# Kernel tuning notes

Hardware: AMD Instinct MI355X
Metric: run time of the kernel (lower is better)

The kernel has to match this reference:

```python
import jax, jax.numpy as jnp
import numpy as np

NEG_SLOPE = 0.2

def gat_layer(x, W, al, ar, src, dst, n_dst):
    # x: [Ns, Fin]; W: [Fin, H*D]; al/ar: [H, D]; src/dst: [E]
    H, D = al.shape
    h = (x @ W).reshape(-1, H, D)          # [Ns, H, D]
    h_dst = h[:n_dst]                       # dst nodes are prefix of src nodes (DGL block)
    el = (h * al).sum(-1)                   # [Ns, H]
    er = (h_dst * ar).sum(-1)               # [Nd, H]
    e = jax.nn.leaky_relu(el[src] + er[dst], NEG_SLOPE)  # [E, H]
    m = jax.ops.segment_max(e, dst, num_segments=n_dst)  # stable edge-softmax
    a = jnp.exp(e - m[dst])
    s = jax.ops.segment_sum(a, dst, num_segments=n_dst)
    alpha = a / s[dst]                      # [E, H]
    msg = h[src] * alpha[:, :, None]        # [E, H, D]
    out = jax.ops.segment_sum(msg, dst, num_segments=n_dst)  # [Nd, H, D]
    return out.reshape(n_dst, H * D)


def setup_inputs() -> dict:
    key = jax.random.key(0)
    ks = jax.random.split(key, 16)
    N0, N1, N2, N3 = 200000, 100000, 50000, 25000
    E0, E1, E2 = 1000000, 500000, 250000
    Fin, Dh, H, C = 256, 64, 3, 40
    inp = {}
    inp['x'] = jax.random.normal(ks[0], (N0, Fin), jnp.float32)
    inp['src0'] = jax.random.randint(ks[1], (E0,), 0, N0, jnp.int32)
    inp['dst0'] = jnp.sort(jax.random.randint(ks[2], (E0,), 0, N1, jnp.int32))
    inp['src1'] = jax.random.randint(ks[3], (E1,), 0, N1, jnp.int32)
    inp['dst1'] = jnp.sort(jax.random.randint(ks[4], (E1,), 0, N2, jnp.int32))
    inp['src2'] = jax.random.randint(ks[5], (E2,), 0, N2, jnp.int32)
    inp['dst2'] = jnp.sort(jax.random.randint(ks[6], (E2,), 0, N3, jnp.int32))
    sc = lambda f: np.float32(1.0 / np.sqrt(f))
    inp['W0'] = jax.random.normal(ks[7], (Fin, H * Dh), jnp.float32) * sc(Fin)
    inp['al0'] = jax.random.normal(ks[8], (H, Dh), jnp.float32) * sc(Dh)
    inp['ar0'] = jax.random.normal(ks[9], (H, Dh), jnp.float32) * sc(Dh)
    inp['W1'] = jax.random.normal(ks[10], (H * Dh, H * Dh), jnp.float32) * sc(H * Dh)
    inp['al1'] = jax.random.normal(ks[11], (H, Dh), jnp.float32) * sc(Dh)
    inp['ar1'] = jax.random.normal(ks[12], (H, Dh), jnp.float32) * sc(Dh)
    inp['W2'] = jax.random.normal(ks[13], (H * Dh, C), jnp.float32) * sc(H * Dh)
    inp['al2'] = jax.random.normal(ks[14], (1, C), jnp.float32) * sc(C)
    inp['ar2'] = jax.random.normal(ks[15], (1, C), jnp.float32) * sc(C)
    return inp


def reference(x, src0, dst0, src1, dst1, src2, dst2,
              W0, al0, ar0, W1, al1, ar1, W2, al2, ar2):
    N1, N2, N3 = 100000, 50000, 25000
    h = gat_layer(x, W0, al0, ar0, src0, dst0, N1)
    h = jax.nn.relu(h)  # dropout is identity in eval/deterministic mode
    h = gat_layer(h, W1, al1, ar1, src1, dst1, N2)
    h = jax.nn.relu(h)
    out = gat_layer(h, W2, al2, ar2, src2, dst2, N3)  # [N3, n_classes]
    return out
```

## Files before the change

kernel.cpp:

```cpp
#include <hip/hip_runtime.h>
#include <math.h>

#define DEV_INLINE __device__ __forceinline__

typedef __attribute__((ext_vector_type(8))) short short8v;
typedef __attribute__((ext_vector_type(4))) float float4v;

DEV_INLINE unsigned short f2bf_rtn(float f) {
  unsigned u = __float_as_uint(f);
  u += 0x7FFFu + ((u >> 16) & 1u);
  return (unsigned short)(u >> 16);
}
DEV_INLINE float bf2f(unsigned short s) { return __uint_as_float(((unsigned)s) << 16); }

DEV_INLINE int soff(int row, int oct) { return row * 32 + ((oct ^ (row & 3)) << 3); }

__global__ void conv_w_all(const float* __restrict__ W0, const float* __restrict__ W1,
                           const float* __restrict__ W2, short* __restrict__ w0h,
                           short* __restrict__ w0l, short* __restrict__ w1h,
                           short* __restrict__ w1l, short* __restrict__ w2h,
                           short* __restrict__ w2l) {
  const int S0 = 256 * 192, S1 = 192 * 192, S2 = 192 * 40;
  int idx = blockIdx.x * 256 + threadIdx.x;
  const float* W; short *Wh, *Wl; int K;
  if (idx < S0) { W = W0; Wh = w0h; Wl = w0l; K = 256; }
  else if (idx < S0 + S1) { idx -= S0; W = W1; Wh = w1h; Wl = w1l; K = 192; }
  else if (idx < S0 + S1 + S2) { idx -= S0 + S1; W = W2; Wh = w2h; Wl = w2l; K = 192; }
  else return;
  int n = idx / K, k = idx - n * K;
  int N = (W == W0 || W == W1) ? 192 : 40;
  float w = W[(size_t)k * N + n];
  unsigned short h = f2bf_rtn(w);
  Wh[idx] = (short)h;
  Wl[idx] = (short)f2bf_rtn(w - bf2f(h));
}

__global__ void csr_all(const int* __restrict__ d0, const int* __restrict__ d1,
                        const int* __restrict__ d2, int* __restrict__ o0,
                        int* __restrict__ o1, int* __restrict__ o2,
                        int E0, int E1, int E2, int n1, int n2, int n3) {
  int i = blockIdx.x * 256 + threadIdx.x;
  const int* dst; int* off; int E, nd;
  if (i < E0) { dst = d0; off = o0; E = E0; nd = n1; }
  else if (i < E0 + E1) { i -= E0; dst = d1; off = o1; E = E1; nd = n2; }
  else if (i < E0 + E1 + E2) { i -= E0 + E1; dst = d2; off = o2; E = E2; nd = n3; }
  else return;
  int d = dst[i];
  int p = (i == 0) ? -1 : dst[i - 1];
  for (int q = p + 1; q <= d; ++q) off[q] = i;
  if (i == E - 1)
    for (int q = d + 1; q <= nd; ++q) off[q] = E;
}

template <int NT, int H>
__global__ __launch_bounds__(256) void gemm_fused(
    const float* __restrict__ A, const short* __restrict__ Bth,
    const short* __restrict__ Btl, const float* __restrict__ al,
    const float* __restrict__ ar, float* __restrict__ C,
    float* __restrict__ el, float* __restrict__ er,
    int M, int N, int K, int n_dst) {
  constexpr int BN = NT * 16;
  constexpr int BREP = (BN + 63) / 64;
  constexpr int TPH = NT / H;
  __shared__ short As_h[128 * 32], As_l[128 * 32];
  __shared__ short Bs_h[BN * 32], Bs_l[BN * 32];
  const int tid = threadIdx.x;
  const int w = tid >> 6, lane = tid & 63;
  const int quad = lane >> 4, l16 = lane & 15;
  const int m0 = blockIdx.x * 128;

  float4v acc[2][NT];
#pragma unroll
  for (int mt = 0; mt < 2; ++mt)
#pragma unroll
    for (int nt = 0; nt < NT; ++nt)
#pragma unroll
      for (int r = 0; r < 4; ++r) acc[mt][nt][r] = 0.f;

  const int sr = tid >> 2;
  const int oct = tid & 3;

  for (int k0 = 0; k0 < K; k0 += 32) {
    float4 a0[2], a1[2];
#pragma unroll
    for (int p = 0; p < 2; ++p) {
      int gr = m0 + sr + p * 64;
      if (gr < M) {
        const float* ap = A + (size_t)gr * K + k0 + oct * 8;
        a0[p] = *(const float4*)ap;
        a1[p] = *(const float4*)(ap + 4);
      } else {
        a0[p] = make_float4(0.f, 0.f, 0.f, 0.f);
        a1[p] = a0[p];
      }
    }
    short8v bh[BREP], bl[BREP];
#pragma unroll
    for (int q = 0; q < BREP; ++q) {
      int n = sr + q * 64;
      if (n < BN) {
        if (n < N) {
          bh[q] = *(const short8v*)(Bth + (size_t)n * K + k0 + oct * 8);
          bl[q] = *(const short8v*)(Btl + (size_t)n * K + k0 + oct * 8);
        } else {
#pragma unroll
          for (int j = 0; j < 8; ++j) { bh[q][j] = 0; bl[q][j] = 0; }
        }
      }
    }
    __syncthreads();
#pragma unroll
    for (int p = 0; p < 2; ++p) {
      int r = sr + p * 64;
      float vs[8] = {a0[p].x, a0[p].y, a0[p].z, a0[p].w,
                     a1[p].x, a1[p].y, a1[p].z, a1[p].w};
      short8v hv, lv;
#pragma unroll
      for (int j = 0; j < 8; ++j) {
        unsigned short h = f2bf_rtn(vs[j]);
        hv[j] = (short)h;
        lv[j] = (short)f2bf_rtn(vs[j] - bf2f(h));
      }
      *(short8v*)(As_h + soff(r, oct)) = hv;
      *(short8v*)(As_l + soff(r, oct)) = lv;
    }
#pragma unroll
    for (int q = 0; q < BREP; ++q) {
      int n = sr + q * 64;
      if (n < BN) {
        *(short8v*)(Bs_h + soff(n, oct)) = bh[q];
        *(short8v*)(Bs_l + soff(n, oct)) = bl[q];
      }
    }
    __syncthreads();
    short8v afh[2], afl[2];
#pragma unroll
    for (int mt = 0; mt < 2; ++mt) {
      int row = w * 32 + mt * 16 + l16;
      afh[mt] = *(const short8v*)(As_h + soff(row, quad));
      afl[mt] = *(const short8v*)(As_l + soff(row, quad));
    }
#pragma unroll
    for (int nt = 0; nt < NT; ++nt) {
      int col = nt * 16 + l16;
      short8v bfh = *(const short8v*)(Bs_h + soff(col, quad));
      short8v bfl = *(const short8v*)(Bs_l + soff(col, quad));
#pragma unroll
      for (int mt = 0; mt < 2; ++mt) {
        acc[mt][nt] = __builtin_amdgcn_mfma_f32_16x16x32_bf16(afh[mt], bfh, acc[mt][nt], 0, 0, 0);
        acc[mt][nt] = __builtin_amdgcn_mfma_f32_16x16x32_bf16(afh[mt], bfl, acc[mt][nt], 0, 0, 0);
        acc[mt][nt] = __builtin_amdgcn_mfma_f32_16x16x32_bf16(afl[mt], bfh, acc[mt][nt], 0, 0, 0);
      }
    }
  }

  float av[NT], rv[NT];
#pragma unroll
  for (int nt = 0; nt < NT; ++nt) {
    int col = nt * 16 + l16;
    av[nt] = (col < N) ? al[col] : 0.f;
    rv[nt] = (col < N) ? ar[col] : 0.f;
  }
#pragma unroll
  for (int mt = 0; mt < 2; ++mt)
#pragma unroll
    for (int r = 0; r < 4; ++r) {
      int gm = m0 + w * 32 + mt * 16 + quad * 4 + r;
      if (gm >= M) continue;
      float pl[H], pr[H];
#pragma unroll
      for (int h = 0; h < H; ++h) { pl[h] = 0.f; pr[h] = 0.f; }
#pragma unroll
      for (int nt = 0; nt < NT; ++nt) {
        int h = nt / TPH;
        pl[h] = fmaf(acc[mt][nt][r], av[nt], pl[h]);
        pr[h] = fmaf(acc[mt][nt][r], rv[nt], pr[h]);
      }
#pragma unroll
      for (int h = 0; h < H; ++h) {
#pragma unroll
        for (int o = 8; o >= 1; o >>= 1) {
          pl[h] += __shfl_xor(pl[h], o, 16);
          pr[h] += __shfl_xor(pr[h], o, 16);
        }
      }
      if (l16 == 0) {
#pragma unroll
        for (int h = 0; h < H; ++h) {
          el[gm * H + h] = pl[h];
          if (gm < n_dst) er[gm * H + h] = pr[h];
        }
      }
#pragma unroll
      for (int nt = 0; nt < NT; ++nt) {
        int col = nt * 16 + l16;
        if (col < N) C[(size_t)gm * N + col] = acc[mt][nt][r];
      }
    }
}

template <int H, int D, bool RELU>
__global__ __launch_bounds__(256) void agg2_kernel(
    const float* __restrict__ hsrc, const float* __restrict__ el,
    const float* __restrict__ er, const int* __restrict__ src,
    const int* __restrict__ off, float* __restrict__ out, int n_dst) {
  constexpr int F = H * D;
  constexpr int NP = (F + 63) / 64;
  __shared__ float wbuf[16][16][H];
  __shared__ int sbuf[16][16];
  const int g = threadIdx.x >> 4, l = threadIdx.x & 15;
  const int d = blockIdx.x * 16 + g;
  if (d >= n_dst) return;
  const int lo = off[d], hi = off[d + 1];

  if (hi <= lo) {
#pragma unroll
    for (int p = 0; p < NP; ++p) {
      int c4 = (p * 16 + l) * 4;
      if (c4 < F) *(float4*)(out + (size_t)d * F + c4) = make_float4(0.f, 0.f, 0.f, 0.f);
    }
    return;
  }

  float erv[H], s_part[H];
#pragma unroll
  for (int h = 0; h < H; ++h) {
    erv[h] = er[d * H + h];
    s_part[h] = 0.f;
  }
  float4 acc[NP];
#pragma unroll
  for (int p = 0; p < NP; ++p) acc[p] = make_float4(0.f, 0.f, 0.f, 0.f);

  for (int base = lo; base < hi; base += 16) {
    const int i = base + l;
    const bool valid = i < hi;
    const int sid = valid ? src[i] : 0;
#pragma unroll
    for (int h = 0; h < H; ++h) {
      float e = 0.f;
      if (valid) {
        e = el[sid * H + h] + erv[h];
        e = e > 0.f ? e : 0.2f * e;
        e = __expf(e);
      }
      s_part[h] += e;
      wbuf[g][l][h] = e;
    }
    sbuf[g][l] = sid;

    const int cnt = min(16, hi - base);
    int sj = sbuf[g][0];
    float4 hv[NP], hn[NP];
#pragma unroll
    for (int p = 0; p < NP; ++p) {
      int c4 = (p * 16 + l) * 4;
      hv[p] = (c4 < F) ? *(const float4*)(hsrc + (size_t)sj * F + c4)
                       : make_float4(0.f, 0.f, 0.f, 0.f);
    }
    for (int ei = 0; ei < cnt; ++ei) {
      if (ei + 1 < cnt) {
        int sj2 = sbuf[g][ei + 1];
#pragma unroll
        for (int p = 0; p < NP; ++p) {
          int c4 = (p * 16 + l) * 4;
          hn[p] = (c4 < F) ? *(const float4*)(hsrc + (size_t)sj2 * F + c4)
                           : make_float4(0.f, 0.f, 0.f, 0.f);
        }
      }
#pragma unroll
      for (int p = 0; p < NP; ++p) {
        int c4 = (p * 16 + l) * 4;
        float wc = wbuf[g][ei][c4 / D];
        acc[p].x = fmaf(wc, hv[p].x, acc[p].x);
        acc[p].y = fmaf(wc, hv[p].y, acc[p].y);
        acc[p].z = fmaf(wc, hv[p].z, acc[p].z);
        acc[p].w = fmaf(wc, hv[p].w, acc[p].w);
      }
#pragma unroll
      for (int p = 0; p < NP; ++p) hv[p] = hn[p];
    }
  }

#pragma unroll
  for (int h = 0; h < H; ++h)
#pragma unroll
    for (int o = 8; o >= 1; o >>= 1) s_part[h] += __shfl_xor(s_part[h], o, 16);

#pragma unroll
  for (int p = 0; p < NP; ++p) {
    int c4 = (p * 16 + l) * 4;
    if (c4 < F) {
      float inv = 1.f / s_part[c4 / D];
      float4 o;
      o.x = acc[p].x * inv; o.y = acc[p].y * inv;
      o.z = acc[p].z * inv; o.w = acc[p].w * inv;
      if (RELU) {
        o.x = fmaxf(o.x, 0.f); o.y = fmaxf(o.y, 0.f);
        o.z = fmaxf(o.z, 0.f); o.w = fmaxf(o.w, 0.f);
      }
      *(float4*)(out + (size_t)d * F + c4) = o;
    }
  }
}

extern "C" void kernel_launch(void* const* d_in, const int* in_sizes, int n_in,
                              void* d_out, int out_size, void* d_ws, size_t ws_size,
                              hipStream_t stream) {
  const float* x   = (const float*)d_in[0];
  const int* src0  = (const int*)d_in[1];
  const int* dst0  = (const int*)d_in[2];
  const int* src1  = (const int*)d_in[3];
  const int* dst1  = (const int*)d_in[4];
  const int* src2  = (const int*)d_in[5];
  const int* dst2  = (const int*)d_in[6];
  const float* W0  = (const float*)d_in[7];
  const float* al0 = (const float*)d_in[8];
  const float* ar0 = (const float*)d_in[9];
  const float* W1  = (const float*)d_in[10];
  const float* al1 = (const float*)d_in[11];
  const float* ar1 = (const float*)d_in[12];
  const float* W2  = (const float*)d_in[13];
  const float* al2 = (const float*)d_in[14];
  const float* ar2 = (const float*)d_in[15];

  const int N0 = 200000, N1 = 100000, N2 = 50000, N3 = 25000;
  const int E0 = in_sizes[1], E1 = in_sizes[3], E2 = in_sizes[5];
  const int Fin = 256, F = 192, C = 40;

  float* ws     = (float*)d_ws;
  float* h_buf  = ws;
  float* o_buf  = h_buf + (size_t)N0 * F;
  float* el_buf = o_buf + (size_t)N1 * F;
  float* er_buf = el_buf + (size_t)N0 * 3;
  short* w0h    = (short*)(er_buf + (size_t)N1 * 3);
  short* w0l    = w0h + 192 * 256;
  short* w1h    = w0l + 192 * 256;
  short* w1l    = w1h + 192 * 192;
  short* w2h    = w1l + 192 * 192;
  short* w2l    = w2h + 40 * 192;
  int*   off0   = (int*)(w2l + 40 * 192);
  int*   off1   = off0 + (N1 + 1);
  int*   off2   = off1 + (N2 + 1);

  dim3 blk(256);

  const int WTOT = 256 * 192 + 192 * 192 + 192 * 40;
  conv_w_all<<<dim3((WTOT + 255) / 256), blk, 0, stream>>>(W0, W1, W2, w0h, w0l, w1h, w1l, w2h, w2l);
  const int ETOT = E0 + E1 + E2;
  csr_all<<<dim3((ETOT + 255) / 256), blk, 0, stream>>>(dst0, dst1, dst2, off0, off1, off2,
                                                        E0, E1, E2, N1, N2, N3);

  gemm_fused<12, 3><<<dim3((N0 + 127) / 128), blk, 0, stream>>>(
      x, w0h, w0l, al0, ar0, h_buf, el_buf, er_buf, N0, F, Fin, N1);
  agg2_kernel<3, 64, true><<<dim3((N1 + 15) / 16), blk, 0, stream>>>(
      h_buf, el_buf, er_buf, src0, off0, o_buf, N1);

  gemm_fused<12, 3><<<dim3((N1 + 127) / 128), blk, 0, stream>>>(
      o_buf, w1h, w1l, al1, ar1, h_buf, el_buf, er_buf, N1, F, F, N2);
  agg2_kernel<3, 64, true><<<dim3((N2 + 15) / 16), blk, 0, stream>>>(
      h_buf, el_buf, er_buf, src1, off1, o_buf, N2);

  gemm_fused<3, 1><<<dim3((N2 + 127) / 128), blk, 0, stream>>>(
      o_buf, w2h, w2l, al2, ar2, h_buf, el_buf, er_buf, N2, C, F, N3);
  agg2_kernel<1, 40, false><<<dim3((N3 + 15) / 16), blk, 0, stream>>>(
      h_buf, el_buf, er_buf, src2, off2, (float*)d_out, N3);
}
```

Measured before the change: 643.6 us.

## Emit bf16 hi/lo split from aggregation, deepen gather prefetch, pad el/er stride

The aggregation kernel now writes its output directly as bf16 hi/lo pairs, so the next GEMM loads pre-split operands instead of converting fp32 per tile. The el/er arrays are padded to stride 4, which allows a single float4 load per node. The gather loop prefetches two rows ahead instead of one, and the LDS swizzle and launch bounds are changed. This removes repeated conversion work and cuts scattered scalar loads, at the cost of extra registers and a more complicated template setup.

```diff
diff --git a/kernel.cpp b/kernel.cpp
--- a/kernel.cpp
+++ b/kernel.cpp
@@ -4,6 +4,7 @@
 #define DEV_INLINE __device__ __forceinline__
 
 typedef __attribute__((ext_vector_type(8))) short short8v;
+typedef __attribute__((ext_vector_type(4))) short short4v;
 typedef __attribute__((ext_vector_type(4))) float float4v;
 
 DEV_INLINE unsigned short f2bf_rtn(float f) {
@@ -13,7 +14,9 @@
 }
 DEV_INLINE float bf2f(unsigned short s) { return __uint_as_float(((unsigned)s) << 16); }
 
-DEV_INLINE int soff(int row, int oct) { return row * 32 + ((oct ^ (row & 3)) << 3); }
+DEV_INLINE int soff(int row, int oct) {
+  return row * 32 + (((oct ^ (row >> 1)) & 3) << 3);
+}
 
 __global__ void conv_w_all(const float* __restrict__ W0, const float* __restrict__ W1,
                            const float* __restrict__ W2, short* __restrict__ w0h,
@@ -22,13 +25,12 @@
                            short* __restrict__ w2l) {
   const int S0 = 256 * 192, S1 = 192 * 192, S2 = 192 * 40;
   int idx = blockIdx.x * 256 + threadIdx.x;
-  const float* W; short *Wh, *Wl; int K;
-  if (idx < S0) { W = W0; Wh = w0h; Wl = w0l; K = 256; }
-  else if (idx < S0 + S1) { idx -= S0; W = W1; Wh = w1h; Wl = w1l; K = 192; }
-  else if (idx < S0 + S1 + S2) { idx -= S0 + S1; W = W2; Wh = w2h; Wl = w2l; K = 192; }
+  const float* W; short *Wh, *Wl; int K, N;
+  if (idx < S0) { W = W0; Wh = w0h; Wl = w0l; K = 256; N = 192; }
+  else if (idx < S0 + S1) { idx -= S0; W = W1; Wh = w1h; Wl = w1l; K = 192; N = 192; }
+  else if (idx < S0 + S1 + S2) { idx -= S0 + S1; W = W2; Wh = w2h; Wl = w2l; K = 192; N = 40; }
   else return;
   int n = idx / K, k = idx - n * K;
-  int N = (W == W0 || W == W1) ? 192 : 40;
   float w = W[(size_t)k * N + n];
   unsigned short h = f2bf_rtn(w);
   Wh[idx] = (short)h;
@@ -52,9 +54,10 @@
     for (int q = d + 1; q <= nd; ++q) off[q] = E;
 }
 
-template <int NT, int H>
-__global__ __launch_bounds__(256) void gemm_fused(
-    const float* __restrict__ A, const short* __restrict__ Bth,
+template <int NT, int H, int ELS, bool SPLIT>
+__global__ __launch_bounds__(256, 4) void gemm_fused(
+    const float* __restrict__ A, const short* __restrict__ Ah,
+    const short* __restrict__ Al, const short* __restrict__ Bth,
     const short* __restrict__ Btl, const float* __restrict__ al,
     const float* __restrict__ ar, float* __restrict__ C,
     float* __restrict__ el, float* __restrict__ er,
@@ -81,17 +84,32 @@
   const int oct = tid & 3;
 
   for (int k0 = 0; k0 < K; k0 += 32) {
+    short8v ah_reg[2], al_reg[2];
     float4 a0[2], a1[2];
-#pragma unroll
-    for (int p = 0; p < 2; ++p) {
-      int gr = m0 + sr + p * 64;
-      if (gr < M) {
-        const float* ap = A + (size_t)gr * K + k0 + oct * 8;
-        a0[p] = *(const float4*)ap;
-        a1[p] = *(const float4*)(ap + 4);
-      } else {
-        a0[p] = make_float4(0.f, 0.f, 0.f, 0.f);
-        a1[p] = a0[p];
+    if (SPLIT) {
+#pragma unroll
+      for (int p = 0; p < 2; ++p) {
+        int gr = m0 + sr + p * 64;
+        if (gr < M) {
+          ah_reg[p] = *(const short8v*)(Ah + (size_t)gr * K + k0 + oct * 8);
+          al_reg[p] = *(const short8v*)(Al + (size_t)gr * K + k0 + oct * 8);
+        } else {
+#pragma unroll
+          for (int j = 0; j < 8; ++j) { ah_reg[p][j] = 0; al_reg[p][j] = 0; }
+        }
+      }
+    } else {
+#pragma unroll
+      for (int p = 0; p < 2; ++p) {
+        int gr = m0 + sr + p * 64;
+        if (gr < M) {
+          const float* ap = A + (size_t)gr * K + k0 + oct * 8;
+          a0[p] = *(const float4*)ap;
+          a1[p] = *(const float4*)(ap + 4);
+        } else {
+          a0[p] = make_float4(0.f, 0.f, 0.f, 0.f);
+          a1[p] = a0[p];
+        }
       }
     }
     short8v bh[BREP], bl[BREP];
@@ -112,14 +130,19 @@
 #pragma unroll
     for (int p = 0; p < 2; ++p) {
       int r = sr + p * 64;
-      float vs[8] = {a0[p].x, a0[p].y, a0[p].z, a0[p].w,
-                     a1[p].x, a1[p].y, a1[p].z, a1[p].w};
       short8v hv, lv;
-#pragma unroll
-      for (int j = 0; j < 8; ++j) {
-        unsigned short h = f2bf_rtn(vs[j]);
-        hv[j] = (short)h;
-        lv[j] = (short)f2bf_rtn(vs[j] - bf2f(h));
+      if (SPLIT) {
+        hv = ah_reg[p];
+        lv = al_reg[p];
+      } else {
+        float vs[8] = {a0[p].x, a0[p].y, a0[p].z, a0[p].w,
+                       a1[p].x, a1[p].y, a1[p].z, a1[p].w};
+#pragma unroll
+        for (int j = 0; j < 8; ++j) {
+          unsigned short h = f2bf_rtn(vs[j]);
+          hv[j] = (short)h;
+          lv[j] = (short)f2bf_rtn(vs[j] - bf2f(h));
+        }
       }
       *(short8v*)(As_h + soff(r, oct)) = hv;
       *(short8v*)(As_l + soff(r, oct)) = lv;
@@ -187,8 +210,8 @@
       if (l16 == 0) {
 #pragma unroll
         for (int h = 0; h < H; ++h) {
-          el[gm * H + h] = pl[h];
-          if (gm < n_dst) er[gm * H + h] = pr[h];
+          el[(size_t)gm * ELS + h] = pl[h];
+          if (gm < n_dst) er[(size_t)gm * ELS + h] = pr[h];
         }
       }
 #pragma unroll
@@ -199,11 +222,12 @@
     }
 }
 
-template <int H, int D, bool RELU>
-__global__ __launch_bounds__(256) void agg2_kernel(
+template <int H, int D, int ELS, bool RELU, bool SPLIT_OUT>
+__global__ __launch_bounds__(256) void agg3_kernel(
     const float* __restrict__ hsrc, const float* __restrict__ el,
     const float* __restrict__ er, const int* __restrict__ src,
-    const int* __restrict__ off, float* __restrict__ out, int n_dst) {
+    const int* __restrict__ off, float* __restrict__ outf,
+    short* __restrict__ outh, short* __restrict__ outl, int n_dst) {
   constexpr int F = H * D;
   constexpr int NP = (F + 63) / 64;
   __shared__ float wbuf[16][16][H];
@@ -217,17 +241,31 @@
 #pragma unroll
     for (int p = 0; p < NP; ++p) {
       int c4 = (p * 16 + l) * 4;
-      if (c4 < F) *(float4*)(out + (size_t)d * F + c4) = make_float4(0.f, 0.f, 0.f, 0.f);
+      if (c4 < F) {
+        if (SPLIT_OUT) {
+          short4v z;
+#pragma unroll
+          for (int j = 0; j < 4; ++j) z[j] = 0;
+          *(short4v*)(outh + (size_t)d * F + c4) = z;
+          *(short4v*)(outl + (size_t)d * F + c4) = z;
+        } else {
+          *(float4*)(outf + (size_t)d * F + c4) = make_float4(0.f, 0.f, 0.f, 0.f);
+        }
+      }
     }
     return;
   }
 
   float erv[H], s_part[H];
-#pragma unroll
-  for (int h = 0; h < H; ++h) {
-    erv[h] = er[d * H + h];
-    s_part[h] = 0.f;
-  }
+  if (H == 3) {
+    float4 t = *(const float4*)(er + (size_t)d * ELS);
+    erv[0] = t.x;
+    if (H > 1) { erv[1] = t.y; erv[2] = t.z; }
+  } else {
+    erv[0] = er[(size_t)d * ELS];
+  }
+#pragma unroll
+  for (int h = 0; h < H; ++h) s_part[h] = 0.f;
   float4 acc[NP];
 #pragma unroll
   for (int p = 0; p < NP; ++p) acc[p] = make_float4(0.f, 0.f, 0.f, 0.f);
@@ -236,35 +274,50 @@
     const int i = base + l;
     const bool valid = i < hi;
     const int sid = valid ? src[i] : 0;
+    sbuf[g][l] = sid;
+    float evs[H];
+    if (H == 3) {
+      float4 t = valid ? *(const float4*)(el + (size_t)sid * ELS)
+                       : make_float4(0.f, 0.f, 0.f, 0.f);
+      evs[0] = t.x;
+      if (H > 1) { evs[1] = t.y; evs[2] = t.z; }
+    } else {
+      evs[0] = valid ? el[(size_t)sid * ELS] : 0.f;
+    }
 #pragma unroll
     for (int h = 0; h < H; ++h) {
       float e = 0.f;
       if (valid) {
-        e = el[sid * H + h] + erv[h];
+        e = evs[h] + erv[h];
         e = e > 0.f ? e : 0.2f * e;
         e = __expf(e);
       }
       s_part[h] += e;
       wbuf[g][l][h] = e;
     }
-    sbuf[g][l] = sid;
 
     const int cnt = min(16, hi - base);
-    int sj = sbuf[g][0];
-    float4 hv[NP], hn[NP];
+    float4 h0[NP], h1[NP], h2[NP];
+    const int sj0 = sbuf[g][0];
+    const int sj1 = sbuf[g][cnt > 1 ? 1 : 0];
 #pragma unroll
     for (int p = 0; p < NP; ++p) {
       int c4 = (p * 16 + l) * 4;
-      hv[p] = (c4 < F) ? *(const float4*)(hsrc + (size_t)sj * F + c4)
-                       : make_float4(0.f, 0.f, 0.f, 0.f);
+      if (c4 < F) {
+        h0[p] = *(const float4*)(hsrc + (size_t)sj0 * F + c4);
+        h1[p] = *(const float4*)(hsrc + (size_t)sj1 * F + c4);
+      } else {
+        h0[p] = make_float4(0.f, 0.f, 0.f, 0.f);
+        h1[p] = h0[p];
+      }
     }
     for (int ei = 0; ei < cnt; ++ei) {
-      if (ei + 1 < cnt) {
-        int sj2 = sbuf[g][ei + 1];
+      if (ei + 2 < cnt) {
+        const int sj2 = sbuf[g][ei + 2];
 #pragma unroll
         for (int p = 0; p < NP; ++p) {
           int c4 = (p * 16 + l) * 4;
-          hn[p] = (c4 < F) ? *(const float4*)(hsrc + (size_t)sj2 * F + c4)
+          h2[p] = (c4 < F) ? *(const float4*)(hsrc + (size_t)sj2 * F + c4)
                            : make_float4(0.f, 0.f, 0.f, 0.f);
         }
       }
@@ -272,13 +325,13 @@
       for (int p = 0; p < NP; ++p) {
         int c4 = (p * 16 + l) * 4;
         float wc = wbuf[g][ei][c4 / D];
-        acc[p].x = fmaf(wc, hv[p].x, acc[p].x);
-        acc[p].y = fmaf(wc, hv[p].y, acc[p].y);
-        acc[p].z = fmaf(wc, hv[p].z, acc[p].z);
-        acc[p].w = fmaf(wc, hv[p].w, acc[p].w);
-      }
-#pragma unroll
-      for (int p = 0; p < NP; ++p) hv[p] = hn[p];
+        acc[p].x = fmaf(wc, h0[p].x, acc[p].x);
+        acc[p].y = fmaf(wc, h0[p].y, acc[p].y);
+        acc[p].z = fmaf(wc, h0[p].z, acc[p].z);
+        acc[p].w = fmaf(wc, h0[p].w, acc[p].w);
+      }
+#pragma unroll
+      for (int p = 0; p < NP; ++p) { h0[p] = h1[p]; h1[p] = h2[p]; }
     }
   }
 
@@ -299,7 +352,20 @@
         o.x = fmaxf(o.x, 0.f); o.y = fmaxf(o.y, 0.f);
         o.z = fmaxf(o.z, 0.f); o.w = fmaxf(o.w, 0.f);
       }
-      *(float4*)(out + (size_t)d * F + c4) = o;
+      if (SPLIT_OUT) {
+        float vs[4] = {o.x, o.y, o.z, o.w};
+        short4v sh, sl;
+#pragma unroll
+        for (int j = 0; j < 4; ++j) {
+          unsigned short hh = f2bf_rtn(vs[j]);
+          sh[j] = (short)hh;
+          sl[j] = (short)f2bf_rtn(vs[j] - bf2f(hh));
+        }
+        *(short4v*)(outh + (size_t)d * F + c4) = sh;
+        *(short4v*)(outl + (size_t)d * F + c4) = sl;
+      } else {
+        *(float4*)(outf + (size_t)d * F + c4) = o;
+      }
     }
   }
 }
@@ -330,10 +396,11 @@
 
   float* ws     = (float*)d_ws;
   float* h_buf  = ws;
-  float* o_buf  = h_buf + (size_t)N0 * F;
-  float* el_buf = o_buf + (size_t)N1 * F;
-  float* er_buf = el_buf + (size_t)N0 * 3;
-  short* w0h    = (short*)(er_buf + (size_t)N1 * 3);
+  float* el_buf = h_buf + (size_t)N0 * F;
+  float* er_buf = el_buf + (size_t)N0 * 4;
+  short* o_hi   = (short*)(er_buf + (size_t)N1 * 4);
+  short* o_lo   = o_hi + (size_t)N1 * F;
+  short* w0h    = o_lo + (size_t)N1 * F;
   short* w0l    = w0h + 192 * 256;
   short* w1h    = w0l + 192 * 256;
   short* w1l    = w1h + 192 * 192;
@@ -351,18 +418,18 @@
   csr_all<<<dim3((ETOT + 255) / 256), blk, 0, stream>>>(dst0, dst1, dst2, off0, off1, off2,
                                                         E0, E1, E2, N1, N2, N3);
 
-  gemm_fused<12, 3><<<dim3((N0 + 127) / 128), blk, 0, stream>>>(
-      x, w0h, w0l, al0, ar0, h_buf, el_buf, er_buf, N0, F, Fin, N1);
-  agg2_kernel<3, 64, true><<<dim3((N1 + 15) / 16), blk, 0, stream>>>(
-      h_buf, el_buf, er_buf, src0, off0, o_buf, N1);
-
-  gemm_fused<12, 3><<<dim3((N1 + 127) / 128), blk, 0, stream>>>(
-      o_buf, w1h, w1l, al1, ar1, h_buf, el_buf, er_buf, N1, F, F, N2);
-  agg2_kernel<3, 64, true><<<dim3((N2 + 15) / 16), blk, 0, stream>>>(
-      h_buf, el_buf, er_buf, src1, off1, o_buf, N2);
-
-  gemm_fused<3, 1><<<dim3((N2 + 127) / 128), blk, 0, stream>>>(
-      o_buf, w2h, w2l, al2, ar2, h_buf, el_buf, er_buf, N2, C, F, N3);
-  agg2_kernel<1, 40, false><<<dim3((N3 + 15) / 16), blk, 0, stream>>>(
-      h_buf, el_buf, er_buf, src2, off2, (float*)d_out, N3);
-}
+  gemm_fused<12, 3, 4, false><<<dim3((N0 + 127) / 128), blk, 0, stream>>>(
+      x, nullptr, nullptr, w0h, w0l, al0, ar0, h_buf, el_buf, er_buf, N0, F, Fin, N1);
+  agg3_kernel<3, 64, 4, true, true><<<dim3((N1 + 15) / 16), blk, 0, stream>>>(
+      h_buf, el_buf, er_buf, src0, off0, nullptr, o_hi, o_lo, N1);
+
+  gemm_fused<12, 3, 4, true><<<dim3((N1 + 127) / 128), blk, 0, stream>>>(
+      nullptr, o_hi, o_lo, w1h, w1l, al1, ar1, h_buf, el_buf, er_buf, N1, F, F, N2);
+  agg3_kernel<3, 64, 4, true, true><<<dim3((N2 + 15) / 16), blk, 0, stream>>>(
+      h_buf, el_buf, er_buf, src1, off1, nullptr, o_hi, o_lo, N2);
+
+  gemm_fused<3, 1, 1, true><<<dim3((N2 + 127) / 128), blk, 0, stream>>>(
+      nullptr, o_hi, o_lo, w2h, w2l, al2, ar2, h_buf, el_buf, er_buf, N2, C, F, N3);
+  agg3_kernel<1, 40, 1, false, false><<<dim3((N3 + 15) / 16), blk, 0, stream>>>(
+      h_buf, el_buf, er_buf, src2, off2, (float*)d_out, nullptr, nullptr, N3);
+}
```

Measured after the change: 1.029 ms. 59.9% more time.
